# Optimization experiments

Measured on AMD Instinct MI355X. Metric: run time of the kernel, lower is better.

Reference implementation:

```python
import jax
import jax.numpy as jnp
from jax import lax
import numpy as np

# ---- static RPN config (mirrors init_kwargs) ----
STRIDES = (8, 16)
SIZES = ((32, 32), (16, 16))
SCALES = ((64.0 ** 2,), (128.0 ** 2,))
RATIOS = ((0.5, 1.0, 2.0), (0.5, 1.0, 2.0))
IMAGE_SIZE = (256, 256)
NMS_THRESH = 0.7
POST_NMS_TOP_N = 2000
NUM_LEVELS = 2
TOP_K_PER_LEVEL = POST_NMS_TOP_N // NUM_LEVELS  # padded NMS output slots per level


def _generate_anchors(stride, scales, ratios, size, image_size):
    """Anchors of shape (H*W*A, 4) in (x1,y1,x2,y2), clamped to image."""
    H, W = size
    cy = (np.arange(H, dtype=np.float32) + 0.5) * stride
    cx = (np.arange(W, dtype=np.float32) + 0.5) * stride
    ws, hs = [], []
    for s in scales:
        for r in ratios:
            ws.append(np.sqrt(s / r))
            hs.append(np.sqrt(s * r))
    ws = np.asarray(ws, np.float32)  # [A]
    hs = np.asarray(hs, np.float32)
    cxg, cyg = np.meshgrid(cx, cy)  # [H, W]
    x1 = cxg[..., None] - 0.5 * ws
    y1 = cyg[..., None] - 0.5 * hs
    x2 = cxg[..., None] + 0.5 * ws
    y2 = cyg[..., None] + 0.5 * hs
    a = np.stack([x1, y1, x2, y2], axis=-1)  # [H, W, A, 4]
    a[..., 0] = np.clip(a[..., 0], 0, image_size[0])
    a[..., 1] = np.clip(a[..., 1], 0, image_size[1])
    a[..., 2] = np.clip(a[..., 2], 0, image_size[0])
    a[..., 3] = np.clip(a[..., 3], 0, image_size[1])
    return a.reshape(-1, 4).astype(np.float32)


ANCHORS = [
    _generate_anchors(STRIDES[i], SCALES[i], RATIOS[i], SIZES[i], IMAGE_SIZE)
    for i in range(NUM_LEVELS)
]


def conv2d(x, w, b, padding):
    y = lax.conv_general_dilated(
        x, w, window_strides=(1, 1), padding=padding,
        dimension_numbers=("NCHW", "OIHW", "NCHW"))
    return y + b[None, :, None, None]


def decode_boxes(anchors, deltas):
    """Standard R-CNN box decode. anchors [N,4], deltas [..., N, 4]."""
    wa = anchors[:, 2] - anchors[:, 0]
    ha = anchors[:, 3] - anchors[:, 1]
    cxa = anchors[:, 0] + 0.5 * wa
    cya = anchors[:, 1] + 0.5 * ha
    dx, dy, dw, dh = deltas[..., 0], deltas[..., 1], deltas[..., 2], deltas[..., 3]
    cx = dx * wa + cxa
    cy = dy * ha + cya
    w = jnp.exp(dw) * wa
    h = jnp.exp(dh) * ha
    return jnp.stack([cx - 0.5 * w, cy - 0.5 * h, cx + 0.5 * w, cy + 0.5 * h], axis=-1)


def clamp_boxes(b):
    return jnp.stack([
        jnp.clip(b[..., 0], 0.0, IMAGE_SIZE[0]),
        jnp.clip(b[..., 1], 0.0, IMAGE_SIZE[1]),
        jnp.clip(b[..., 2], 0.0, IMAGE_SIZE[0]),
        jnp.clip(b[..., 3], 0.0, IMAGE_SIZE[1]),
    ], axis=-1)


def _pairwise_iou(b):
    # b: [N, 4] -> [N, N] IoU (torchvision convention, no +1)
    area = (b[:, 2] - b[:, 0]) * (b[:, 3] - b[:, 1])
    lt = jnp.maximum(b[:, None, :2], b[None, :, :2])
    rb = jnp.minimum(b[:, None, 2:], b[None, :, 2:])
    wh = jnp.clip(rb - lt, 0.0)
    inter = wh[..., 0] * wh[..., 1]
    return inter / (area[:, None] + area[None, :] - inter)


def nms_padded(boxes, scores, thresh, top_k):
    """Exact greedy NMS; returns (top_k,4) boxes and (top_k,) scores padded with -1."""
    N = boxes.shape[0]
    order = jnp.argsort(-scores)
    b = boxes[order]
    s = scores[order]
    iou = _pairwise_iou(b)  # [N, N]

    def body(supp, xs):
        row, i = xs
        keep_i = jnp.logical_not(supp[i])
        supp = supp | (keep_i & (row > thresh) & (jnp.arange(N) > i))
        return supp, keep_i

    _, keep = lax.scan(body, jnp.zeros((N,), bool), (iou, jnp.arange(N)))
    rank = jnp.cumsum(keep) - 1  # position among kept, in score order
    slot = jnp.where(keep & (rank < top_k), rank, top_k)  # overflow -> dump row
    out_b = jnp.full((top_k + 1, 4), -1.0, boxes.dtype).at[slot].set(b)
    out_s = jnp.full((top_k + 1,), -1.0, scores.dtype).at[slot].set(s)
    return out_b[:top_k], out_s[:top_k]


def _rpn_level(feat, anchors, conv_w, conv_b, cls_w, cls_b, reg_w, reg_b):
    x = jax.nn.relu(conv2d(feat, conv_w, conv_b, "SAME"))
    cls = conv2d(x, cls_w, cls_b, "VALID")              # [BS, A, H, W]
    reg = conv2d(x, reg_w, reg_b, "VALID")              # [BS, 4A, H, W]
    BS, A, H, W = cls.shape
    cls = cls.transpose(0, 2, 3, 1).reshape(BS, -1)                      # [BS, HWA]
    reg = reg.transpose(0, 2, 3, 1).reshape(BS, H, W, A, 4).reshape(BS, -1, 4)
    boxes = clamp_boxes(decode_boxes(anchors, lax.stop_gradient(reg)))   # [BS, HWA, 4]
    scores = jax.nn.sigmoid(lax.stop_gradient(cls))                      # [BS, HWA]
    kb, ks = jax.vmap(lambda bb, ss: nms_padded(bb, ss, NMS_THRESH, TOP_K_PER_LEVEL))(boxes, scores)
    return kb, ks


def setup_inputs() -> dict:
    key = jax.random.key(0)
    ks = jax.random.split(key, 5)
    C = 256
    A = 3
    return {
        "feat0": jax.random.normal(ks[0], (4, C, 32, 32), jnp.float32),
        "feat1": jax.random.normal(ks[1], (4, C, 16, 16), jnp.float32),
        "conv_w": 0.01 * jax.random.normal(ks[2], (C, C, 3, 3), jnp.float32),
        "conv_b": jnp.zeros((C,), jnp.float32),
        "cls_w": 0.01 * jax.random.normal(ks[3], (A, C, 1, 1), jnp.float32),
        "cls_b": jnp.zeros((A,), jnp.float32),
        "reg_w": 0.01 * jax.random.normal(ks[4], (4 * A, C, 1, 1), jnp.float32),
        "reg_b": jnp.zeros((4 * A,), jnp.float32),
    }


def reference(feat0, feat1, conv_w, conv_b, cls_w, cls_b, reg_w, reg_b):
    feats = [feat0, feat1]
    kb_all, ks_all = [], []
    for i in range(NUM_LEVELS):
        kb, ks = _rpn_level(feats[i], jnp.asarray(ANCHORS[i]),
                            conv_w, conv_b, cls_w, cls_b, reg_w, reg_b)
        kb_all.append(kb)
        ks_all.append(ks)
    bboxes = jnp.concatenate(kb_all, axis=1)   # [BS, POST_NMS_TOP_N, 4]
    scores = jnp.concatenate(ks_all, axis=1)   # [BS, POST_NMS_TOP_N]
    idx = jnp.argsort(-scores, axis=1)         # descending; -1 pads go last
    bboxes = jnp.take_along_axis(bboxes, idx[..., None], axis=1)
    return bboxes
```

## Files before the change

kernel.cpp:

```cpp
#include <hip/hip_runtime.h>
#include <math.h>


__global__ __launch_bounds__(256, 4) void conv3_sk_u(
    const float* __restrict__ feat0, const float* __restrict__ feat1,
    const float* __restrict__ conv_w,
    double* __restrict__ part0, double* __restrict__ part1)
{
  __shared__ float Ald[2][16][64];
  __shared__ float Bld[2][16][64];
  const int t = threadIdx.x;
  const int bid = blockIdx.x;
  const float* feat;
  double* part;
  int oc_t, p_t, k_base, hw_sh, w_sh, H;
  if (bid < 1024) {
    int kc = bid >> 8;
    feat = feat0; part = part0 + (size_t)kc * 4096 * 256;
    oc_t = bid & 3; p_t = (bid >> 2) & 63;
    k_base = kc * 576; hw_sh = 10; w_sh = 5; H = 32;
  } else {
    int b2 = bid - 1024;
    int kc = b2 >> 6;
    feat = feat1; part = part1 + (size_t)kc * 1024 * 256;
    oc_t = b2 & 3; p_t = (b2 >> 2) & 15;
    k_base = kc * 576; hw_sh = 8; w_sh = 4; H = 16;
  }
  const int oc_base = oc_t * 64;
  const int p_base  = p_t * 64;
  const int wmask = H - 1, hwmask = (1 << hw_sh) - 1;
  const int skk = t >> 4;
  const int q4  = (t & 15) * 4;

  float a_r[4], b_r[4];
  auto load_tile = [&](int kt) {
    const int k0 = k_base + kt * 16;
    const float* wrow = conv_w + (size_t)(oc_base + q4) * 2304 + (k0 + skk);
#pragma unroll
    for (int u = 0; u < 4; ++u) a_r[u] = wrow[(size_t)u * 2304];
    int p = p_base + q4;
    int b = p >> hw_sh, pin = p & hwmask;
    int y = pin >> w_sh, x0 = pin & wmask;
    int k = k0 + skk;
    int ic = k / 9, rr = k - ic * 9;
    int ky = rr / 3, kx = rr - ky * 3;
    int iy = y + ky - 1;
    const float* frow = feat + (((b << 8) + ic) << hw_sh) + (iy << w_sh);
    bool yok = (unsigned)iy < (unsigned)H;
#pragma unroll
    for (int u = 0; u < 4; ++u) {
      int ix = x0 + u + kx - 1;
      b_r[u] = (yok && (unsigned)ix < (unsigned)H) ? frow[ix] : 0.f;
    }
  };

  const int ty4 = (t >> 4) * 4;
  const int tx4 = (t & 15) * 4;
  double acc[4][4] = {};

  load_tile(0);
  for (int kt = 0; kt < 36; ++kt) {
    const int buf = kt & 1;
    *(float4*)&Ald[buf][skk][q4] = make_float4(a_r[0], a_r[1], a_r[2], a_r[3]);
    *(float4*)&Bld[buf][skk][q4] = make_float4(b_r[0], b_r[1], b_r[2], b_r[3]);
    __syncthreads();
    if (kt + 1 < 36) load_tile(kt + 1);
#pragma unroll
    for (int kk = 0; kk < 16; ++kk) {
      float4 av = *(const float4*)&Ald[buf][kk][ty4];
      float4 bv = *(const float4*)&Bld[buf][kk][tx4];
      double ad[4] = {(double)av.x, (double)av.y, (double)av.z, (double)av.w};
      double bd[4] = {(double)bv.x, (double)bv.y, (double)bv.z, (double)bv.w};
#pragma unroll
      for (int i = 0; i < 4; ++i)
#pragma unroll
        for (int j = 0; j < 4; ++j) acc[i][j] += ad[i] * bd[j];
    }
  }
#pragma unroll
  for (int j = 0; j < 4; ++j) {
    int p = p_base + tx4 + j;
    double* row = part + (size_t)p * 256 + oc_base + ty4;
    *(double2*)&row[0] = make_double2(acc[0][j], acc[1][j]);
    *(double2*)&row[2] = make_double2(acc[2][j], acc[3][j]);
  }
}

__global__ __launch_bounds__(256) void rhd_k(
    const double* __restrict__ part0, const double* __restrict__ part1,
    const float* __restrict__ conv_b,
    const float* __restrict__ cls_w, const float* __restrict__ cls_b,
    const float* __restrict__ reg_w, const float* __restrict__ reg_b,
    float* __restrict__ box0, float* __restrict__ sc0,
    float* __restrict__ box1, float* __restrict__ sc1)
{
  int wid = (blockIdx.x * 256 + threadIdx.x) >> 6;
  int lane = threadIdx.x & 63;
  int lvl = wid >= 4096;
  const double* part = lvl ? part1 : part0;
  int p = lvl ? wid - 4096 : wid;
  int M = lvl ? 1024 : 4096;
  double s4[4];
  {
    float4 bv = ((const float4*)conv_b)[lane];
    s4[0] = (double)bv.x; s4[1] = (double)bv.y;
    s4[2] = (double)bv.z; s4[3] = (double)bv.w;
  }
#pragma unroll
  for (int ks = 0; ks < 4; ++ks) {
    const double2* pr = (const double2*)(part + (size_t)ks * M * 256 + (size_t)p * 256);
    double2 a = pr[2 * lane], b = pr[2 * lane + 1];
    s4[0] += a.x; s4[1] += a.y; s4[2] += b.x; s4[3] += b.y;
  }
  float xv[4];
#pragma unroll
  for (int q = 0; q < 4; ++q) {
    float f = (float)s4[q];
    xv[q] = f > 0.f ? f : 0.f;
  }
  double acc[15];
#pragma unroll
  for (int o = 0; o < 15; ++o) {
    const float* wr = (o < 3) ? (cls_w + o * 256) : (reg_w + (o - 3) * 256);
    float4 wv = ((const float4*)wr)[lane];
    acc[o] = (double)wv.x * (double)xv[0] + (double)wv.y * (double)xv[1] +
             (double)wv.z * (double)xv[2] + (double)wv.w * (double)xv[3];
  }
#pragma unroll
  for (int d = 1; d < 64; d <<= 1)
#pragma unroll
    for (int o = 0; o < 15; ++o)
      acc[o] += __shfl_xor(acc[o], d, 64);
  if (lane < 3) {
    int a = lane;
    float cls = (float)(acc[a] + (double)cls_b[a]);
    float score = 1.f / (1.f + expf(-cls));
    float dx = (float)(acc[3 + a * 4 + 0] + (double)reg_b[a * 4 + 0]);
    float dy = (float)(acc[3 + a * 4 + 1] + (double)reg_b[a * 4 + 1]);
    float dw = (float)(acc[3 + a * 4 + 2] + (double)reg_b[a * 4 + 2]);
    float dh = (float)(acc[3 + a * 4 + 3] + (double)reg_b[a * 4 + 3]);
    int hw_sh = lvl ? 8 : 10, w_sh = lvl ? 4 : 5, Wd = lvl ? 16 : 32;
    float S = lvl ? 16.f : 8.f;
    double scale = lvl ? 16384.0 : 4096.0;
    int b = p >> hw_sh, pin = p & ((1 << hw_sh) - 1);
    int y = pin >> w_sh, x = pin & (Wd - 1);
    double ratio = (a == 0) ? 0.5 : (a == 1 ? 1.0 : 2.0);
    float w_a = (float)sqrt(scale / ratio);
    float h_a = (float)sqrt(scale * ratio);
    float cx = ((float)x + 0.5f) * S;
    float cy = ((float)y + 0.5f) * S;
    float x1 = cx - 0.5f * w_a, y1 = cy - 0.5f * h_a;
    float x2 = cx + 0.5f * w_a, y2 = cy + 0.5f * h_a;
    x1 = fminf(fmaxf(x1, 0.f), 256.f); y1 = fminf(fmaxf(y1, 0.f), 256.f);
    x2 = fminf(fmaxf(x2, 0.f), 256.f); y2 = fminf(fmaxf(y2, 0.f), 256.f);
    float wa = x2 - x1, ha = y2 - y1;
    float cxa = x1 + 0.5f * wa, cya = y1 + 0.5f * ha;
    float ncx = dx * wa + cxa;
    float ncy = dy * ha + cya;
    float nw = expf(dw) * wa;
    float nh = expf(dh) * ha;
    float bx1 = ncx - 0.5f * nw, by1 = ncy - 0.5f * nh;
    float bx2 = ncx + 0.5f * nw, by2 = ncy + 0.5f * nh;
    bx1 = fminf(fmaxf(bx1, 0.f), 256.f); by1 = fminf(fmaxf(by1, 0.f), 256.f);
    bx2 = fminf(fmaxf(bx2, 0.f), 256.f); by2 = fminf(fmaxf(by2, 0.f), 256.f);
    int n = pin * 3 + a;
    if (lvl) {
      ((float4*)box1)[(size_t)b * 768 + n] = make_float4(bx1, by1, bx2, by2);
      sc1[b * 768 + n] = score;
    } else {
      ((float4*)box0)[(size_t)b * 3072 + n] = make_float4(bx1, by1, bx2, by2);
      sc0[b * 3072 + n] = score;
    }
  }
}

__global__ __launch_bounds__(256) void sort_level_k(
    const float* __restrict__ sc0, const float* __restrict__ box0,
    float* __restrict__ ssc0, float* __restrict__ sbox0,
    const float* __restrict__ sc1, const float* __restrict__ box1,
    float* __restrict__ ssc1, float* __restrict__ sbox1)
{
  __shared__ __align__(16) float s[3072];
  int z = blockIdx.x;
  const float *sc, *box; float *ssc, *sbox; int N, b, c;
  if (z < 48) { sc = sc0; box = box0; ssc = ssc0; sbox = sbox0; N = 3072; b = z / 12; c = z % 12; }
  else { int z2 = z - 48; sc = sc1; box = box1; ssc = ssc1; sbox = sbox1; N = 768; b = z2 / 3; c = z2 % 3; }
  const float* scb = sc + (size_t)b * N;
  for (int j = threadIdx.x; j < N; j += 256) s[j] = scb[j];
  __syncthreads();
  int i = c * 256 + threadIdx.x;
  float si = s[i];
  int rank = 0;
  const float4* sv = (const float4*)s;
  for (int j4 = 0; j4 < (N >> 2); ++j4) {
    float4 v = sv[j4];
    int j = j4 * 4;
    rank += (v.x > si) || (v.x == si && (j + 0) < i);
    rank += (v.y > si) || (v.y == si && (j + 1) < i);
    rank += (v.z > si) || (v.z == si && (j + 2) < i);
    rank += (v.w > si) || (v.w == si && (j + 3) < i);
  }
  ssc[(size_t)b * N + rank] = si;
  float4 bi = ((const float4*)box)[(size_t)b * N + i];
  ((float4*)sbox)[(size_t)b * N + rank] = bi;
}

__global__ __launch_bounds__(256) void mask_col_k(
    const float* __restrict__ sbox0, const float* __restrict__ sbox1,
    unsigned long long* __restrict__ mask0, unsigned long long* __restrict__ mask1,
    unsigned long long* __restrict__ colD0, unsigned long long* __restrict__ colD1)
{
  int bid = blockIdx.x;
  if (bid < 2448) {
    __shared__ float4 bj[64];
    const float* sbox; unsigned long long* mask; int N, words, w, i_ch, b;
    if (bid < 2304) {
      sbox = sbox0; mask = mask0; N = 3072; words = 48;
      w = bid % 48; int r = bid / 48; i_ch = r % 12; b = r / 12;
    } else {
      int z = bid - 2304;
      sbox = sbox1; mask = mask1; N = 768; words = 12;
      w = z % 12; int r = z / 12; i_ch = r % 3; b = r / 3;
    }
    int i = i_ch * 256 + threadIdx.x;
    if (threadIdx.x < 64)
      bj[threadIdx.x] = ((const float4*)sbox)[(size_t)b * N + w * 64 + threadIdx.x];
    __syncthreads();
    float4 bi = ((const float4*)sbox)[(size_t)b * N + i];
    float ai = (bi.z - bi.x) * (bi.w - bi.y);
    unsigned long long m = 0ull;
#pragma unroll 16
    for (int jj = 0; jj < 64; ++jj) {
      int j = w * 64 + jj;
      float4 bv = bj[jj];
      float lx = fmaxf(bi.x, bv.x), ly = fmaxf(bi.y, bv.y);
      float rx = fminf(bi.z, bv.z), ry = fminf(bi.w, bv.w);
      float iw = fmaxf(rx - lx, 0.f), ih = fmaxf(ry - ly, 0.f);
      float inter = iw * ih;
      float aj = (bv.z - bv.x) * (bv.w - bv.y);
      float iou = inter / (ai + aj - inter);
      if ((iou > 0.7f) & (j > i)) m |= (1ull << jj);
    }
    mask[((size_t)b * N + i) * words + w] = m;
  } else {
    __shared__ float4 tb[4][64];
    int sub = threadIdx.x >> 6, lane = threadIdx.x & 63;
    const float* sbox; unsigned long long* colD; int N, tile, b;
    if (bid < 2496) {
      int unit = (bid - 2448) * 4 + sub;
      sbox = sbox0; colD = colD0; N = 3072;
      tile = unit % 48; b = unit / 48;
    } else {
      int unit = (bid - 2496) * 4 + sub;
      sbox = sbox1; colD = colD1; N = 768;
      tile = unit % 12; b = unit / 12;
    }
    tb[sub][lane] = ((const float4*)sbox)[(size_t)b * N + tile * 64 + lane];
    __syncthreads();
    float4 bq = tb[sub][lane];
    float aq = (bq.z - bq.x) * (bq.w - bq.y);
    unsigned long long col = 0ull;
#pragma unroll 16
    for (int ii = 0; ii < 64; ++ii) {
      float4 bi = tb[sub][ii];
      float lx = fmaxf(bq.x, bi.x), ly = fmaxf(bq.y, bi.y);
      float rx = fminf(bq.z, bi.z), ry = fminf(bq.w, bi.w);
      float iw = fmaxf(rx - lx, 0.f), ih = fmaxf(ry - ly, 0.f);
      float inter = iw * ih;
      float ai = (bi.z - bi.x) * (bi.w - bi.y);
      float iou = inter / (aq + ai - inter);
      if ((iou > 0.7f) & (lane > ii)) col |= (1ull << ii);
    }
    colD[(size_t)b * N + tile * 64 + lane] = col;
  }
}

__global__ __launch_bounds__(64) void nms_scan_k(
    const float* __restrict__ ssc0, const float* __restrict__ sbox0,
    const unsigned long long* __restrict__ mask0,
    const unsigned long long* __restrict__ colD0,
    const float* __restrict__ ssc1, const float* __restrict__ sbox1,
    const unsigned long long* __restrict__ mask1,
    const unsigned long long* __restrict__ colD1,
    float* __restrict__ cb, float* __restrict__ cs)
{
  int z = blockIdx.x;
  int lvl = z >> 2, b = z & 3;
  int N = lvl ? 768 : 3072;
  int words = lvl ? 12 : 48;
  const float* ssc = (lvl ? ssc1 : ssc0) + (size_t)b * N;
  const float4* sbox = ((const float4*)(lvl ? sbox1 : sbox0)) + (size_t)b * N;
  const unsigned long long* mask = (lvl ? mask1 : mask0) + (size_t)b * N * words;
  const unsigned long long* colD = (lvl ? colD1 : colD0) + (size_t)b * N;
  const int lane = threadIdx.x;
  float* csb = cs + (size_t)b * 2000 + lvl * 1000;
  float4* cbb = (float4*)(cb + ((size_t)b * 2000 + lvl * 1000) * 4);
  for (int q = lane; q < 1000; q += 64) {
    csb[q] = -1.f;
    cbb[q] = make_float4(-1.f, -1.f, -1.f, -1.f);
  }
  unsigned long long removed = 0ull;
  int kept_base = 0;
  unsigned long long colv = colD[lane];
  float sc_i = ssc[lane];
  float4 bx_i = sbox[lane];
  for (int t = 0; t < words; ++t) {
    unsigned long long wr = __shfl(removed, t);
    bool doprop = (lane > t) && (lane < words);
    const unsigned long long* row = mask + (size_t)t * 64 * words + lane;
    unsigned long long v1[32], v2[32];
    if (doprop) {
#pragma unroll
      for (int s = 0; s < 32; ++s) v1[s] = row[(size_t)s * words];
#pragma unroll
      for (int s = 0; s < 32; ++s) v2[s] = row[(size_t)(32 + s) * words];
    }
    bool rm = (wr >> lane) & 1ull;
    bool kp = false;
    unsigned long long Rv = wr;
    unsigned long long Kv = 0ull;
    while (true) {
      bool F = (!rm) && (!kp) && ((colv & ~Rv) == 0ull);
      unsigned long long Fv = __ballot(F);
      if (Fv == 0ull) break;
      kp = kp || F;
      Kv |= Fv;
      bool newr = (!rm) && (!kp) && ((colv & Fv) != 0ull);
      rm = rm || newr;
      Rv = __ballot(rm);
    }
    unsigned long long keep64 = Kv;
    if (kp) {
      int rank = kept_base + __popcll(keep64 & ((1ull << lane) - 1ull));
      if (rank < 1000) { csb[rank] = sc_i; cbb[rank] = bx_i; }
    }
    kept_base += __popcll(keep64);
    if (kept_base >= 1000) break;
    if (t + 1 >= words) break;
    {
      int i2 = (t + 1) * 64 + lane;
      colv = colD[i2]; sc_i = ssc[i2]; bx_i = sbox[i2];
    }
    if (doprop) {
      unsigned long long acc = removed;
#pragma unroll
      for (int s = 0; s < 32; ++s)
        acc |= (((keep64 >> s) & 1ull) ? v1[s] : 0ull);
#pragma unroll
      for (int s = 0; s < 32; ++s)
        acc |= (((keep64 >> (32 + s)) & 1ull) ? v2[s] : 0ull);
      removed = acc;
    }
  }
}

__global__ __launch_bounds__(256) void final_sort_k(
    const float* __restrict__ cs, const float* __restrict__ cb,
    float* __restrict__ out)
{
  __shared__ __align__(16) float s[2000];
  int b = blockIdx.x >> 3, c = blockIdx.x & 7;
  const float* csb = cs + (size_t)b * 2000;
  for (int j = threadIdx.x; j < 2000; j += 256) s[j] = csb[j];
  __syncthreads();
  if (threadIdx.x >= 250) return;
  int li = c * 250 + threadIdx.x;
  float si = s[li];
  int rank = 0;
  const float4* sv = (const float4*)s;
  for (int j4 = 0; j4 < 500; ++j4) {
    float4 v = sv[j4];
    int j = j4 * 4;
    rank += (v.x > si) || (v.x == si && (j + 0) < li);
    rank += (v.y > si) || (v.y == si && (j + 1) < li);
    rank += (v.z > si) || (v.z == si && (j + 2) < li);
    rank += (v.w > si) || (v.w == si && (j + 3) < li);
  }
  float4 bi = ((const float4*)cb)[(size_t)b * 2000 + li];
  ((float4*)out)[(size_t)b * 2000 + rank] = bi;
}

extern "C" void kernel_launch(void* const* d_in, const int* in_sizes, int n_in,
                              void* d_out, int out_size, void* d_ws, size_t ws_size,
                              hipStream_t stream) {
  const float* feat0  = (const float*)d_in[0];
  const float* feat1  = (const float*)d_in[1];
  const float* conv_w = (const float*)d_in[2];
  const float* conv_b = (const float*)d_in[3];
  const float* cls_w  = (const float*)d_in[4];
  const float* cls_b  = (const float*)d_in[5];
  const float* reg_w  = (const float*)d_in[6];
  const float* reg_b  = (const float*)d_in[7];

  char* p = (char*)d_ws;
  auto alloc = [&](size_t bytes) {
    char* r = p;
    p += (bytes + 255) & ~(size_t)255;
    return r;
  };
  double* part0 = (double*)alloc((size_t)4 * 4096 * 256 * 8);
  double* part1 = (double*)alloc((size_t)4 * 1024 * 256 * 8);
  float* box0 = (float*)alloc((size_t)4 * 3072 * 16);
  float* sc0  = (float*)alloc((size_t)4 * 3072 * 4);
  float* box1 = (float*)alloc((size_t)4 * 768 * 16);
  float* sc1  = (float*)alloc((size_t)4 * 768 * 4);
  float* sbox0 = (float*)alloc((size_t)4 * 3072 * 16);
  float* ssc0  = (float*)alloc((size_t)4 * 3072 * 4);
  float* sbox1 = (float*)alloc((size_t)4 * 768 * 16);
  float* ssc1  = (float*)alloc((size_t)4 * 768 * 4);
  unsigned long long* mask0 = (unsigned long long*)alloc((size_t)4 * 3072 * 48 * 8);
  unsigned long long* mask1 = (unsigned long long*)alloc((size_t)4 * 768 * 12 * 8);
  unsigned long long* colD0 = (unsigned long long*)alloc((size_t)4 * 3072 * 8);
  unsigned long long* colD1 = (unsigned long long*)alloc((size_t)4 * 768 * 8);
  float* cb = (float*)alloc((size_t)4 * 2000 * 16);
  float* cs = (float*)alloc((size_t)4 * 2000 * 4);

  conv3_sk_u<<<1280, 256, 0, stream>>>(feat0, feat1, conv_w, part0, part1);
  rhd_k<<<1280, 256, 0, stream>>>(part0, part1, conv_b, cls_w, cls_b,
                                  reg_w, reg_b, box0, sc0, box1, sc1);
  sort_level_k<<<60, 256, 0, stream>>>(sc0, box0, ssc0, sbox0,
                                       sc1, box1, ssc1, sbox1);
  mask_col_k<<<2508, 256, 0, stream>>>(sbox0, sbox1, mask0, mask1, colD0, colD1);
  nms_scan_k<<<8, 64, 0, stream>>>(ssc0, sbox0, mask0, colD0,
                                   ssc1, sbox1, mask1, colD1, cb, cs);
  final_sort_k<<<32, 256, 0, stream>>>(cs, cb, (float*)d_out);
}
```

Baseline: 533.2 us.

## Fuse post-conv stages into one persistent kernel with grid barriers

Merges the head, per-level sort, IoU mask, NMS scan and final sort kernels into a single persistent kernel of 512 blocks, separated by software grid barriers built on atomics. The aim is to remove per-kernel launch overhead and the gaps between the five small dependent launches. In exchange it adds a memset and barrier spin costs. It also relies on all 512 blocks being resident at once (launch bounds 256,2), since otherwise the barrier deadlocks. The NMS scan now loads its mask rows in two halves to reduce register use.

```diff
diff --git a/kernel.cpp b/kernel.cpp
--- a/kernel.cpp
+++ b/kernel.cpp
@@ -86,298 +86,305 @@
   }
 }
 
-__global__ __launch_bounds__(256) void rhd_k(
+#define POST_NBLK 512
+__device__ __forceinline__ void grid_barrier(int* cnt, int* gen) {
+  __syncthreads();
+  if (threadIdx.x == 0) {
+    __threadfence();
+    int g = atomicAdd(gen, 0);
+    if (atomicAdd(cnt, 1) == POST_NBLK - 1) {
+      atomicExch(cnt, 0);
+      __threadfence();
+      atomicAdd(gen, 1);
+    } else {
+      while (atomicAdd(gen, 0) == g) { __builtin_amdgcn_s_sleep(8); }
+    }
+    __threadfence();
+  }
+  __syncthreads();
+}
+
+__global__ __launch_bounds__(256, 2) void post_k(
     const double* __restrict__ part0, const double* __restrict__ part1,
     const float* __restrict__ conv_b,
     const float* __restrict__ cls_w, const float* __restrict__ cls_b,
     const float* __restrict__ reg_w, const float* __restrict__ reg_b,
-    float* __restrict__ box0, float* __restrict__ sc0,
-    float* __restrict__ box1, float* __restrict__ sc1)
+    float* box0, float* sc0, float* box1, float* sc1,
+    float* ssc0, float* sbox0, float* ssc1, float* sbox1,
+    unsigned long long* mask0, unsigned long long* mask1,
+    unsigned long long* colD0, unsigned long long* colD1,
+    float* cb, float* cs, float* out, int* bar)
 {
-  int wid = (blockIdx.x * 256 + threadIdx.x) >> 6;
-  int lane = threadIdx.x & 63;
-  int lvl = wid >= 4096;
-  const double* part = lvl ? part1 : part0;
-  int p = lvl ? wid - 4096 : wid;
-  int M = lvl ? 1024 : 4096;
-  double s4[4];
-  {
-    float4 bv = ((const float4*)conv_b)[lane];
-    s4[0] = (double)bv.x; s4[1] = (double)bv.y;
-    s4[2] = (double)bv.z; s4[3] = (double)bv.w;
-  }
-#pragma unroll
-  for (int ks = 0; ks < 4; ++ks) {
-    const double2* pr = (const double2*)(part + (size_t)ks * M * 256 + (size_t)p * 256);
-    double2 a = pr[2 * lane], b = pr[2 * lane + 1];
-    s4[0] += a.x; s4[1] += a.y; s4[2] += b.x; s4[3] += b.y;
-  }
-  float xv[4];
-#pragma unroll
-  for (int q = 0; q < 4; ++q) {
-    float f = (float)s4[q];
-    xv[q] = f > 0.f ? f : 0.f;
-  }
-  double acc[15];
-#pragma unroll
-  for (int o = 0; o < 15; ++o) {
-    const float* wr = (o < 3) ? (cls_w + o * 256) : (reg_w + (o - 3) * 256);
-    float4 wv = ((const float4*)wr)[lane];
-    acc[o] = (double)wv.x * (double)xv[0] + (double)wv.y * (double)xv[1] +
-             (double)wv.z * (double)xv[2] + (double)wv.w * (double)xv[3];
-  }
-#pragma unroll
-  for (int d = 1; d < 64; d <<= 1)
-#pragma unroll
-    for (int o = 0; o < 15; ++o)
-      acc[o] += __shfl_xor(acc[o], d, 64);
-  if (lane < 3) {
-    int a = lane;
-    float cls = (float)(acc[a] + (double)cls_b[a]);
-    float score = 1.f / (1.f + expf(-cls));
-    float dx = (float)(acc[3 + a * 4 + 0] + (double)reg_b[a * 4 + 0]);
-    float dy = (float)(acc[3 + a * 4 + 1] + (double)reg_b[a * 4 + 1]);
-    float dw = (float)(acc[3 + a * 4 + 2] + (double)reg_b[a * 4 + 2]);
-    float dh = (float)(acc[3 + a * 4 + 3] + (double)reg_b[a * 4 + 3]);
-    int hw_sh = lvl ? 8 : 10, w_sh = lvl ? 4 : 5, Wd = lvl ? 16 : 32;
-    float S = lvl ? 16.f : 8.f;
-    double scale = lvl ? 16384.0 : 4096.0;
-    int b = p >> hw_sh, pin = p & ((1 << hw_sh) - 1);
-    int y = pin >> w_sh, x = pin & (Wd - 1);
-    double ratio = (a == 0) ? 0.5 : (a == 1 ? 1.0 : 2.0);
-    float w_a = (float)sqrt(scale / ratio);
-    float h_a = (float)sqrt(scale * ratio);
-    float cx = ((float)x + 0.5f) * S;
-    float cy = ((float)y + 0.5f) * S;
-    float x1 = cx - 0.5f * w_a, y1 = cy - 0.5f * h_a;
-    float x2 = cx + 0.5f * w_a, y2 = cy + 0.5f * h_a;
-    x1 = fminf(fmaxf(x1, 0.f), 256.f); y1 = fminf(fmaxf(y1, 0.f), 256.f);
-    x2 = fminf(fmaxf(x2, 0.f), 256.f); y2 = fminf(fmaxf(y2, 0.f), 256.f);
-    float wa = x2 - x1, ha = y2 - y1;
-    float cxa = x1 + 0.5f * wa, cya = y1 + 0.5f * ha;
-    float ncx = dx * wa + cxa;
-    float ncy = dy * ha + cya;
-    float nw = expf(dw) * wa;
-    float nh = expf(dh) * ha;
-    float bx1 = ncx - 0.5f * nw, by1 = ncy - 0.5f * nh;
-    float bx2 = ncx + 0.5f * nw, by2 = ncy + 0.5f * nh;
-    bx1 = fminf(fmaxf(bx1, 0.f), 256.f); by1 = fminf(fmaxf(by1, 0.f), 256.f);
-    bx2 = fminf(fmaxf(bx2, 0.f), 256.f); by2 = fminf(fmaxf(by2, 0.f), 256.f);
-    int n = pin * 3 + a;
-    if (lvl) {
-      ((float4*)box1)[(size_t)b * 768 + n] = make_float4(bx1, by1, bx2, by2);
-      sc1[b * 768 + n] = score;
+  int* bcnt = bar;
+  int* bgen = bar + 1;
+  __shared__ __align__(16) float smem[3072];
+  const int bid = blockIdx.x;
+  const int tid = threadIdx.x;
+  const int lane = tid & 63;
+
+  for (int u = bid * 4 + (tid >> 6); u < 5120; u += 2048) {
+    int lvl = u >= 4096;
+    const double* part = lvl ? part1 : part0;
+    int p = lvl ? u - 4096 : u;
+    int M = lvl ? 1024 : 4096;
+    double s4[4];
+    {
+      float4 bv = ((const float4*)conv_b)[lane];
+      s4[0] = (double)bv.x; s4[1] = (double)bv.y;
+      s4[2] = (double)bv.z; s4[3] = (double)bv.w;
+    }
+#pragma unroll
+    for (int ks = 0; ks < 4; ++ks) {
+      const double2* pr = (const double2*)(part + (size_t)ks * M * 256 + (size_t)p * 256);
+      double2 a = pr[2 * lane], b = pr[2 * lane + 1];
+      s4[0] += a.x; s4[1] += a.y; s4[2] += b.x; s4[3] += b.y;
+    }
+    float xv[4];
+#pragma unroll
+    for (int q = 0; q < 4; ++q) {
+      float f = (float)s4[q];
+      xv[q] = f > 0.f ? f : 0.f;
+    }
+    double acc[15];
+#pragma unroll
+    for (int o = 0; o < 15; ++o) {
+      const float* wr = (o < 3) ? (cls_w + o * 256) : (reg_w + (o - 3) * 256);
+      float4 wv = ((const float4*)wr)[lane];
+      acc[o] = (double)wv.x * (double)xv[0] + (double)wv.y * (double)xv[1] +
+               (double)wv.z * (double)xv[2] + (double)wv.w * (double)xv[3];
+    }
+#pragma unroll
+    for (int d = 1; d < 64; d <<= 1)
+#pragma unroll
+      for (int o = 0; o < 15; ++o)
+        acc[o] += __shfl_xor(acc[o], d, 64);
+    if (lane < 3) {
+      int a = lane;
+      float cls = (float)(acc[a] + (double)cls_b[a]);
+      float score = 1.f / (1.f + expf(-cls));
+      float dx = (float)(acc[3 + a * 4 + 0] + (double)reg_b[a * 4 + 0]);
+      float dy = (float)(acc[3 + a * 4 + 1] + (double)reg_b[a * 4 + 1]);
+      float dw = (float)(acc[3 + a * 4 + 2] + (double)reg_b[a * 4 + 2]);
+      float dh = (float)(acc[3 + a * 4 + 3] + (double)reg_b[a * 4 + 3]);
+      int hw_sh = lvl ? 8 : 10, w_sh = lvl ? 4 : 5, Wd = lvl ? 16 : 32;
+      float S = lvl ? 16.f : 8.f;
+      double scale = lvl ? 16384.0 : 4096.0;
+      int b = p >> hw_sh, pin = p & ((1 << hw_sh) - 1);
+      int y = pin >> w_sh, x = pin & (Wd - 1);
+      double ratio = (a == 0) ? 0.5 : (a == 1 ? 1.0 : 2.0);
+      float w_a = (float)sqrt(scale / ratio);
+      float h_a = (float)sqrt(scale * ratio);
+      float cx = ((float)x + 0.5f) * S;
+      float cy = ((float)y + 0.5f) * S;
+      float x1 = cx - 0.5f * w_a, y1 = cy - 0.5f * h_a;
+      float x2 = cx + 0.5f * w_a, y2 = cy + 0.5f * h_a;
+      x1 = fminf(fmaxf(x1, 0.f), 256.f); y1 = fminf(fmaxf(y1, 0.f), 256.f);
+      x2 = fminf(fmaxf(x2, 0.f), 256.f); y2 = fminf(fmaxf(y2, 0.f), 256.f);
+      float wa = x2 - x1, ha = y2 - y1;
+      float cxa = x1 + 0.5f * wa, cya = y1 + 0.5f * ha;
+      float ncx = dx * wa + cxa;
+      float ncy = dy * ha + cya;
+      float nw = expf(dw) * wa;
+      float nh = expf(dh) * ha;
+      float bx1 = ncx - 0.5f * nw, by1 = ncy - 0.5f * nh;
+      float bx2 = ncx + 0.5f * nw, by2 = ncy + 0.5f * nh;
+      bx1 = fminf(fmaxf(bx1, 0.f), 256.f); by1 = fminf(fmaxf(by1, 0.f), 256.f);
+      bx2 = fminf(fmaxf(bx2, 0.f), 256.f); by2 = fminf(fmaxf(by2, 0.f), 256.f);
+      int n = pin * 3 + a;
+      if (lvl) {
+        ((float4*)box1)[(size_t)b * 768 + n] = make_float4(bx1, by1, bx2, by2);
+        sc1[b * 768 + n] = score;
+      } else {
+        ((float4*)box0)[(size_t)b * 3072 + n] = make_float4(bx1, by1, bx2, by2);
+        sc0[b * 3072 + n] = score;
+      }
+    }
+  }
+  grid_barrier(bcnt, bgen);
+
+  if (bid < 60) {
+    const float *sc, *box; float *ssc, *sbox; int N, b, c;
+    if (bid < 48) { sc = sc0; box = box0; ssc = ssc0; sbox = sbox0; N = 3072; b = bid / 12; c = bid % 12; }
+    else { int z2 = bid - 48; sc = sc1; box = box1; ssc = ssc1; sbox = sbox1; N = 768; b = z2 / 3; c = z2 % 3; }
+    const float* scb = sc + (size_t)b * N;
+    for (int j = tid; j < N; j += 256) smem[j] = scb[j];
+    __syncthreads();
+    int i = c * 256 + tid;
+    float si = smem[i];
+    int rank = 0;
+    const float4* sv = (const float4*)smem;
+    for (int j4 = 0; j4 < (N >> 2); ++j4) {
+      float4 v = sv[j4];
+      int j = j4 * 4;
+      rank += (v.x > si) || (v.x == si && (j + 0) < i);
+      rank += (v.y > si) || (v.y == si && (j + 1) < i);
+      rank += (v.z > si) || (v.z == si && (j + 2) < i);
+      rank += (v.w > si) || (v.w == si && (j + 3) < i);
+    }
+    ssc[(size_t)b * N + rank] = si;
+    float4 bi = ((const float4*)box)[(size_t)b * N + i];
+    ((float4*)sbox)[(size_t)b * N + rank] = bi;
+  }
+  grid_barrier(bcnt, bgen);
+
+  for (int u = bid; u < 2508; u += 512) {
+    __syncthreads();
+    float4* f4 = (float4*)smem;
+    if (u < 2448) {
+      const float* sbox; unsigned long long* mask; int N, words, w, i_ch, b;
+      if (u < 2304) {
+        sbox = sbox0; mask = mask0; N = 3072; words = 48;
+        w = u % 48; int r = u / 48; i_ch = r % 12; b = r / 12;
+      } else {
+        int z = u - 2304;
+        sbox = sbox1; mask = mask1; N = 768; words = 12;
+        w = z % 12; int r = z / 12; i_ch = r % 3; b = r / 3;
+      }
+      int i = i_ch * 256 + tid;
+      if (tid < 64)
+        f4[tid] = ((const float4*)sbox)[(size_t)b * N + w * 64 + tid];
+      __syncthreads();
+      float4 bi = ((const float4*)sbox)[(size_t)b * N + i];
+      float ai = (bi.z - bi.x) * (bi.w - bi.y);
+      unsigned long long m = 0ull;
+#pragma unroll 16
+      for (int jj = 0; jj < 64; ++jj) {
+        int j = w * 64 + jj;
+        float4 bv = f4[jj];
+        float lx = fmaxf(bi.x, bv.x), ly = fmaxf(bi.y, bv.y);
+        float rx = fminf(bi.z, bv.z), ry = fminf(bi.w, bv.w);
+        float iw = fmaxf(rx - lx, 0.f), ih = fmaxf(ry - ly, 0.f);
+        float inter = iw * ih;
+        float aj = (bv.z - bv.x) * (bv.w - bv.y);
+        float iou = inter / (ai + aj - inter);
+        if ((iou > 0.7f) & (j > i)) m |= (1ull << jj);
+      }
+      mask[((size_t)b * N + i) * words + w] = m;
     } else {
-      ((float4*)box0)[(size_t)b * 3072 + n] = make_float4(bx1, by1, bx2, by2);
-      sc0[b * 3072 + n] = score;
-    }
-  }
-}
-
-__global__ __launch_bounds__(256) void sort_level_k(
-    const float* __restrict__ sc0, const float* __restrict__ box0,
-    float* __restrict__ ssc0, float* __restrict__ sbox0,
-    const float* __restrict__ sc1, const float* __restrict__ box1,
-    float* __restrict__ ssc1, float* __restrict__ sbox1)
-{
-  __shared__ __align__(16) float s[3072];
-  int z = blockIdx.x;
-  const float *sc, *box; float *ssc, *sbox; int N, b, c;
-  if (z < 48) { sc = sc0; box = box0; ssc = ssc0; sbox = sbox0; N = 3072; b = z / 12; c = z % 12; }
-  else { int z2 = z - 48; sc = sc1; box = box1; ssc = ssc1; sbox = sbox1; N = 768; b = z2 / 3; c = z2 % 3; }
-  const float* scb = sc + (size_t)b * N;
-  for (int j = threadIdx.x; j < N; j += 256) s[j] = scb[j];
-  __syncthreads();
-  int i = c * 256 + threadIdx.x;
-  float si = s[i];
-  int rank = 0;
-  const float4* sv = (const float4*)s;
-  for (int j4 = 0; j4 < (N >> 2); ++j4) {
-    float4 v = sv[j4];
-    int j = j4 * 4;
-    rank += (v.x > si) || (v.x == si && (j + 0) < i);
-    rank += (v.y > si) || (v.y == si && (j + 1) < i);
-    rank += (v.z > si) || (v.z == si && (j + 2) < i);
-    rank += (v.w > si) || (v.w == si && (j + 3) < i);
-  }
-  ssc[(size_t)b * N + rank] = si;
-  float4 bi = ((const float4*)box)[(size_t)b * N + i];
-  ((float4*)sbox)[(size_t)b * N + rank] = bi;
-}
-
-__global__ __launch_bounds__(256) void mask_col_k(
-    const float* __restrict__ sbox0, const float* __restrict__ sbox1,
-    unsigned long long* __restrict__ mask0, unsigned long long* __restrict__ mask1,
-    unsigned long long* __restrict__ colD0, unsigned long long* __restrict__ colD1)
-{
-  int bid = blockIdx.x;
-  if (bid < 2448) {
-    __shared__ float4 bj[64];
-    const float* sbox; unsigned long long* mask; int N, words, w, i_ch, b;
-    if (bid < 2304) {
-      sbox = sbox0; mask = mask0; N = 3072; words = 48;
-      w = bid % 48; int r = bid / 48; i_ch = r % 12; b = r / 12;
-    } else {
-      int z = bid - 2304;
-      sbox = sbox1; mask = mask1; N = 768; words = 12;
-      w = z % 12; int r = z / 12; i_ch = r % 3; b = r / 3;
-    }
-    int i = i_ch * 256 + threadIdx.x;
-    if (threadIdx.x < 64)
-      bj[threadIdx.x] = ((const float4*)sbox)[(size_t)b * N + w * 64 + threadIdx.x];
+      int sub = tid >> 6;
+      const float* sbox; unsigned long long* colD; int N, tile, b;
+      if (u < 2496) {
+        int unit = (u - 2448) * 4 + sub;
+        sbox = sbox0; colD = colD0; N = 3072;
+        tile = unit % 48; b = unit / 48;
+      } else {
+        int unit = (u - 2496) * 4 + sub;
+        sbox = sbox1; colD = colD1; N = 768;
+        tile = unit % 12; b = unit / 12;
+      }
+      f4[sub * 64 + lane] = ((const float4*)sbox)[(size_t)b * N + tile * 64 + lane];
+      __syncthreads();
+      float4 bq = f4[sub * 64 + lane];
+      float aq = (bq.z - bq.x) * (bq.w - bq.y);
+      unsigned long long col = 0ull;
+#pragma unroll 16
+      for (int ii = 0; ii < 64; ++ii) {
+        float4 bi = f4[sub * 64 + ii];
+        float lx = fmaxf(bq.x, bi.x), ly = fmaxf(bq.y, bi.y);
+        float rx = fminf(bq.z, bi.z), ry = fminf(bq.w, bi.w);
+        float iw = fmaxf(rx - lx, 0.f), ih = fmaxf(ry - ly, 0.f);
+        float inter = iw * ih;
+        float ai = (bi.z - bi.x) * (bi.w - bi.y);
+        float iou = inter / (aq + ai - inter);
+        if ((iou > 0.7f) & (lane > ii)) col |= (1ull << ii);
+      }
+      colD[(size_t)b * N + tile * 64 + lane] = col;
+    }
+  }
+  grid_barrier(bcnt, bgen);
+
+  if (bid < 8 && tid < 64) {
+    int lvl = bid >> 2, b = bid & 3;
+    int N = lvl ? 768 : 3072;
+    int words = lvl ? 12 : 48;
+    const float* ssc = (lvl ? ssc1 : ssc0) + (size_t)b * N;
+    const float4* sbox = ((const float4*)(lvl ? sbox1 : sbox0)) + (size_t)b * N;
+    const unsigned long long* mask = (lvl ? mask1 : mask0) + (size_t)b * N * words;
+    const unsigned long long* colD = (lvl ? colD1 : colD0) + (size_t)b * N;
+    float* csb = cs + (size_t)b * 2000 + lvl * 1000;
+    float4* cbb = (float4*)(cb + ((size_t)b * 2000 + lvl * 1000) * 4);
+    for (int q = lane; q < 1000; q += 64) {
+      csb[q] = -1.f;
+      cbb[q] = make_float4(-1.f, -1.f, -1.f, -1.f);
+    }
+    unsigned long long removed = 0ull;
+    int kept_base = 0;
+    unsigned long long colv = colD[lane];
+    float sc_i = ssc[lane];
+    float4 bx_i = sbox[lane];
+    for (int t = 0; t < words; ++t) {
+      unsigned long long wr = __shfl(removed, t);
+      bool doprop = (lane > t) && (lane < words);
+      const unsigned long long* row = mask + (size_t)t * 64 * words + lane;
+      unsigned long long v[32];
+      if (doprop) {
+#pragma unroll
+        for (int s = 0; s < 32; ++s) v[s] = row[(size_t)s * words];
+      }
+      bool rm = (wr >> lane) & 1ull;
+      bool kp = false;
+      unsigned long long Rv = wr;
+      unsigned long long Kv = 0ull;
+      while (true) {
+        bool F = (!rm) && (!kp) && ((colv & ~Rv) == 0ull);
+        unsigned long long Fv = __ballot(F);
+        if (Fv == 0ull) break;
+        kp = kp || F;
+        Kv |= Fv;
+        bool newr = (!rm) && (!kp) && ((colv & Fv) != 0ull);
+        rm = rm || newr;
+        Rv = __ballot(rm);
+      }
+      unsigned long long keep64 = Kv;
+      if (kp) {
+        int rank = kept_base + __popcll(keep64 & ((1ull << lane) - 1ull));
+        if (rank < 1000) { csb[rank] = sc_i; cbb[rank] = bx_i; }
+      }
+      kept_base += __popcll(keep64);
+      if (kept_base >= 1000) break;
+      if (t + 1 >= words) break;
+      {
+        int i2 = (t + 1) * 64 + lane;
+        colv = colD[i2]; sc_i = ssc[i2]; bx_i = sbox[i2];
+      }
+      if (doprop) {
+        unsigned long long acc = removed;
+#pragma unroll
+        for (int s = 0; s < 32; ++s)
+          acc |= (((keep64 >> s) & 1ull) ? v[s] : 0ull);
+#pragma unroll
+        for (int s = 0; s < 32; ++s) v[s] = row[(size_t)(32 + s) * words];
+#pragma unroll
+        for (int s = 0; s < 32; ++s)
+          acc |= (((keep64 >> (32 + s)) & 1ull) ? v[s] : 0ull);
+        removed = acc;
+      }
+    }
+  }
+  grid_barrier(bcnt, bgen);
+
+  if (bid < 32) {
+    int b = bid >> 3, c = bid & 7;
+    const float* csb = cs + (size_t)b * 2000;
+    for (int j = tid; j < 2000; j += 256) smem[j] = csb[j];
     __syncthreads();
-    float4 bi = ((const float4*)sbox)[(size_t)b * N + i];
-    float ai = (bi.z - bi.x) * (bi.w - bi.y);
-    unsigned long long m = 0ull;
-#pragma unroll 16
-    for (int jj = 0; jj < 64; ++jj) {
-      int j = w * 64 + jj;
-      float4 bv = bj[jj];
-      float lx = fmaxf(bi.x, bv.x), ly = fmaxf(bi.y, bv.y);
-      float rx = fminf(bi.z, bv.z), ry = fminf(bi.w, bv.w);
-      float iw = fmaxf(rx - lx, 0.f), ih = fmaxf(ry - ly, 0.f);
-      float inter = iw * ih;
-      float aj = (bv.z - bv.x) * (bv.w - bv.y);
-      float iou = inter / (ai + aj - inter);
-      if ((iou > 0.7f) & (j > i)) m |= (1ull << jj);
-    }
-    mask[((size_t)b * N + i) * words + w] = m;
-  } else {
-    __shared__ float4 tb[4][64];
-    int sub = threadIdx.x >> 6, lane = threadIdx.x & 63;
-    const float* sbox; unsigned long long* colD; int N, tile, b;
-    if (bid < 2496) {
-      int unit = (bid - 2448) * 4 + sub;
-      sbox = sbox0; colD = colD0; N = 3072;
-      tile = unit % 48; b = unit / 48;
-    } else {
-      int unit = (bid - 2496) * 4 + sub;
-      sbox = sbox1; colD = colD1; N = 768;
-      tile = unit % 12; b = unit / 12;
-    }
-    tb[sub][lane] = ((const float4*)sbox)[(size_t)b * N + tile * 64 + lane];
-    __syncthreads();
-    float4 bq = tb[sub][lane];
-    float aq = (bq.z - bq.x) * (bq.w - bq.y);
-    unsigned long long col = 0ull;
-#pragma unroll 16
-    for (int ii = 0; ii < 64; ++ii) {
-      float4 bi = tb[sub][ii];
-      float lx = fmaxf(bq.x, bi.x), ly = fmaxf(bq.y, bi.y);
-      float rx = fminf(bq.z, bi.z), ry = fminf(bq.w, bi.w);
-      float iw = fmaxf(rx - lx, 0.f), ih = fmaxf(ry - ly, 0.f);
-      float inter = iw * ih;
-      float ai = (bi.z - bi.x) * (bi.w - bi.y);
-      float iou = inter / (aq + ai - inter);
-      if ((iou > 0.7f) & (lane > ii)) col |= (1ull << ii);
-    }
-    colD[(size_t)b * N + tile * 64 + lane] = col;
-  }
-}
-
-__global__ __launch_bounds__(64) void nms_scan_k(
-    const float* __restrict__ ssc0, const float* __restrict__ sbox0,
-    const unsigned long long* __restrict__ mask0,
-    const unsigned long long* __restrict__ colD0,
-    const float* __restrict__ ssc1, const float* __restrict__ sbox1,
-    const unsigned long long* __restrict__ mask1,
-    const unsigned long long* __restrict__ colD1,
-    float* __restrict__ cb, float* __restrict__ cs)
-{
-  int z = blockIdx.x;
-  int lvl = z >> 2, b = z & 3;
-  int N = lvl ? 768 : 3072;
-  int words = lvl ? 12 : 48;
-  const float* ssc = (lvl ? ssc1 : ssc0) + (size_t)b * N;
-  const float4* sbox = ((const float4*)(lvl ? sbox1 : sbox0)) + (size_t)b * N;
-  const unsigned long long* mask = (lvl ? mask1 : mask0) + (size_t)b * N * words;
-  const unsigned long long* colD = (lvl ? colD1 : colD0) + (size_t)b * N;
-  const int lane = threadIdx.x;
-  float* csb = cs + (size_t)b * 2000 + lvl * 1000;
-  float4* cbb = (float4*)(cb + ((size_t)b * 2000 + lvl * 1000) * 4);
-  for (int q = lane; q < 1000; q += 64) {
-    csb[q] = -1.f;
-    cbb[q] = make_float4(-1.f, -1.f, -1.f, -1.f);
-  }
-  unsigned long long removed = 0ull;
-  int kept_base = 0;
-  unsigned long long colv = colD[lane];
-  float sc_i = ssc[lane];
-  float4 bx_i = sbox[lane];
-  for (int t = 0; t < words; ++t) {
-    unsigned long long wr = __shfl(removed, t);
-    bool doprop = (lane > t) && (lane < words);
-    const unsigned long long* row = mask + (size_t)t * 64 * words + lane;
-    unsigned long long v1[32], v2[32];
-    if (doprop) {
-#pragma unroll
-      for (int s = 0; s < 32; ++s) v1[s] = row[(size_t)s * words];
-#pragma unroll
-      for (int s = 0; s < 32; ++s) v2[s] = row[(size_t)(32 + s) * words];
-    }
-    bool rm = (wr >> lane) & 1ull;
-    bool kp = false;
-    unsigned long long Rv = wr;
-    unsigned long long Kv = 0ull;
-    while (true) {
-      bool F = (!rm) && (!kp) && ((colv & ~Rv) == 0ull);
-      unsigned long long Fv = __ballot(F);
-      if (Fv == 0ull) break;
-      kp = kp || F;
-      Kv |= Fv;
-      bool newr = (!rm) && (!kp) && ((colv & Fv) != 0ull);
-      rm = rm || newr;
-      Rv = __ballot(rm);
-    }
-    unsigned long long keep64 = Kv;
-    if (kp) {
-      int rank = kept_base + __popcll(keep64 & ((1ull << lane) - 1ull));
-      if (rank < 1000) { csb[rank] = sc_i; cbb[rank] = bx_i; }
-    }
-    kept_base += __popcll(keep64);
-    if (kept_base >= 1000) break;
-    if (t + 1 >= words) break;
-    {
-      int i2 = (t + 1) * 64 + lane;
-      colv = colD[i2]; sc_i = ssc[i2]; bx_i = sbox[i2];
-    }
-    if (doprop) {
-      unsigned long long acc = removed;
-#pragma unroll
-      for (int s = 0; s < 32; ++s)
-        acc |= (((keep64 >> s) & 1ull) ? v1[s] : 0ull);
-#pragma unroll
-      for (int s = 0; s < 32; ++s)
-        acc |= (((keep64 >> (32 + s)) & 1ull) ? v2[s] : 0ull);
-      removed = acc;
-    }
-  }
-}
-
-__global__ __launch_bounds__(256) void final_sort_k(
-    const float* __restrict__ cs, const float* __restrict__ cb,
-    float* __restrict__ out)
-{
-  __shared__ __align__(16) float s[2000];
-  int b = blockIdx.x >> 3, c = blockIdx.x & 7;
-  const float* csb = cs + (size_t)b * 2000;
-  for (int j = threadIdx.x; j < 2000; j += 256) s[j] = csb[j];
-  __syncthreads();
-  if (threadIdx.x >= 250) return;
-  int li = c * 250 + threadIdx.x;
-  float si = s[li];
-  int rank = 0;
-  const float4* sv = (const float4*)s;
-  for (int j4 = 0; j4 < 500; ++j4) {
-    float4 v = sv[j4];
-    int j = j4 * 4;
-    rank += (v.x > si) || (v.x == si && (j + 0) < li);
-    rank += (v.y > si) || (v.y == si && (j + 1) < li);
-    rank += (v.z > si) || (v.z == si && (j + 2) < li);
-    rank += (v.w > si) || (v.w == si && (j + 3) < li);
-  }
-  float4 bi = ((const float4*)cb)[(size_t)b * 2000 + li];
-  ((float4*)out)[(size_t)b * 2000 + rank] = bi;
+    if (tid < 250) {
+      int li = c * 250 + tid;
+      float si = smem[li];
+      int rank = 0;
+      const float4* sv = (const float4*)smem;
+      for (int j4 = 0; j4 < 500; ++j4) {
+        float4 v = sv[j4];
+        int j = j4 * 4;
+        rank += (v.x > si) || (v.x == si && (j + 0) < li);
+        rank += (v.y > si) || (v.y == si && (j + 1) < li);
+        rank += (v.z > si) || (v.z == si && (j + 2) < li);
+        rank += (v.w > si) || (v.w == si && (j + 3) < li);
+      }
+      float4 bi = ((const float4*)cb)[(size_t)b * 2000 + li];
+      ((float4*)out)[(size_t)b * 2000 + rank] = bi;
+    }
+  }
 }
 
 extern "C" void kernel_launch(void* const* d_in, const int* in_sizes, int n_in,
@@ -414,14 +421,13 @@
   unsigned long long* colD1 = (unsigned long long*)alloc((size_t)4 * 768 * 8);
   float* cb = (float*)alloc((size_t)4 * 2000 * 16);
   float* cs = (float*)alloc((size_t)4 * 2000 * 4);
+  int* bar = (int*)alloc(256);
+  float* outp = (float*)d_out;
 
   conv3_sk_u<<<1280, 256, 0, stream>>>(feat0, feat1, conv_w, part0, part1);
-  rhd_k<<<1280, 256, 0, stream>>>(part0, part1, conv_b, cls_w, cls_b,
-                                  reg_w, reg_b, box0, sc0, box1, sc1);
-  sort_level_k<<<60, 256, 0, stream>>>(sc0, box0, ssc0, sbox0,
-                                       sc1, box1, ssc1, sbox1);
-  mask_col_k<<<2508, 256, 0, stream>>>(sbox0, sbox1, mask0, mask1, colD0, colD1);
-  nms_scan_k<<<8, 64, 0, stream>>>(ssc0, sbox0, mask0, colD0,
-                                   ssc1, sbox1, mask1, colD1, cb, cs);
-  final_sort_k<<<32, 256, 0, stream>>>(cs, cb, (float*)d_out);
+  hipMemsetAsync(bar, 0, 8, stream);
+  post_k<<<POST_NBLK, 256, 0, stream>>>(
+      part0, part1, conv_b, cls_w, cls_b, reg_w, reg_b,
+      box0, sc0, box1, sc1, ssc0, sbox0, ssc1, sbox1,
+      mask0, mask1, colD0, colD1, cb, cs, outp, bar);
 }
```

Result: slower. 697.6 us (+30.8%).

## Split NMS mask propagation across four waves with shared-memory reduction

Applied to the files above, without the earlier changes.

The serial NMS scan kernel now runs 256 threads per block instead of one 64-lane wave. Each wave loads 16 of the 64 mask rows per tile, so per-thread register pressure and load latency drop. Wave 0 alone runs the greedy keep/remove ballot loop. All waves then OR their partial suppression masks into shared memory, which adds three block barriers per tile in exchange for spreading the mask loads.

```diff
diff --git a/kernel.cpp b/kernel.cpp
--- a/kernel.cpp
+++ b/kernel.cpp
@@ -275,7 +275,7 @@
   }
 }
 
-__global__ __launch_bounds__(64) void nms_scan_k(
+__global__ __launch_bounds__(256) void nms_scan_k(
     const float* __restrict__ ssc0, const float* __restrict__ sbox0,
     const unsigned long long* __restrict__ mask0,
     const unsigned long long* __restrict__ colD0,
@@ -292,65 +292,81 @@
   const float4* sbox = ((const float4*)(lvl ? sbox1 : sbox0)) + (size_t)b * N;
   const unsigned long long* mask = (lvl ? mask1 : mask0) + (size_t)b * N * words;
   const unsigned long long* colD = (lvl ? colD1 : colD0) + (size_t)b * N;
-  const int lane = threadIdx.x;
+  const int tid = threadIdx.x;
+  const int lane = tid & 63;
+  const int wv = tid >> 6;
   float* csb = cs + (size_t)b * 2000 + lvl * 1000;
   float4* cbb = (float4*)(cb + ((size_t)b * 2000 + lvl * 1000) * 4);
-  for (int q = lane; q < 1000; q += 64) {
+
+  __shared__ unsigned long long rem[48];
+  __shared__ unsigned long long part[4][64];
+  __shared__ unsigned long long keepSh;
+  __shared__ int doneSh;
+
+  if (tid < 48) rem[tid] = 0ull;
+  if (tid == 0) doneSh = 0;
+  for (int q = tid; q < 1000; q += 256) {
     csb[q] = -1.f;
     cbb[q] = make_float4(-1.f, -1.f, -1.f, -1.f);
   }
-  unsigned long long removed = 0ull;
+  unsigned long long colv = 0ull; float sc_i = 0.f; float4 bx_i;
+  if (wv == 0) { colv = colD[lane]; sc_i = ssc[lane]; bx_i = sbox[lane]; }
   int kept_base = 0;
-  unsigned long long colv = colD[lane];
-  float sc_i = ssc[lane];
-  float4 bx_i = sbox[lane];
+  __syncthreads();
+
   for (int t = 0; t < words; ++t) {
-    unsigned long long wr = __shfl(removed, t);
-    bool doprop = (lane > t) && (lane < words);
-    const unsigned long long* row = mask + (size_t)t * 64 * words + lane;
-    unsigned long long v1[32], v2[32];
-    if (doprop) {
-#pragma unroll
-      for (int s = 0; s < 32; ++s) v1[s] = row[(size_t)s * words];
-#pragma unroll
-      for (int s = 0; s < 32; ++s) v2[s] = row[(size_t)(32 + s) * words];
-    }
-    bool rm = (wr >> lane) & 1ull;
-    bool kp = false;
-    unsigned long long Rv = wr;
-    unsigned long long Kv = 0ull;
-    while (true) {
-      bool F = (!rm) && (!kp) && ((colv & ~Rv) == 0ull);
-      unsigned long long Fv = __ballot(F);
-      if (Fv == 0ull) break;
-      kp = kp || F;
-      Kv |= Fv;
-      bool newr = (!rm) && (!kp) && ((colv & Fv) != 0ull);
-      rm = rm || newr;
-      Rv = __ballot(rm);
-    }
-    unsigned long long keep64 = Kv;
-    if (kp) {
-      int rank = kept_base + __popcll(keep64 & ((1ull << lane) - 1ull));
-      if (rank < 1000) { csb[rank] = sc_i; cbb[rank] = bx_i; }
-    }
-    kept_base += __popcll(keep64);
-    if (kept_base >= 1000) break;
-    if (t + 1 >= words) break;
-    {
-      int i2 = (t + 1) * 64 + lane;
-      colv = colD[i2]; sc_i = ssc[i2]; bx_i = sbox[i2];
-    }
-    if (doprop) {
-      unsigned long long acc = removed;
-#pragma unroll
-      for (int s = 0; s < 32; ++s)
-        acc |= (((keep64 >> s) & 1ull) ? v1[s] : 0ull);
-#pragma unroll
-      for (int s = 0; s < 32; ++s)
-        acc |= (((keep64 >> (32 + s)) & 1ull) ? v2[s] : 0ull);
-      removed = acc;
-    }
+    unsigned long long v[16];
+    if (lane < words) {
+      const unsigned long long* rowb =
+          mask + ((size_t)t * 64 + wv * 16) * words + lane;
+#pragma unroll
+      for (int s = 0; s < 16; ++s) v[s] = rowb[(size_t)s * words];
+    }
+    if (wv == 0) {
+      unsigned long long wr = rem[t];
+      bool rm = (wr >> lane) & 1ull;
+      bool kp = false;
+      unsigned long long Rv = wr;
+      unsigned long long Kv = 0ull;
+      while (true) {
+        bool F = (!rm) && (!kp) && ((colv & ~Rv) == 0ull);
+        unsigned long long Fv = __ballot(F);
+        if (Fv == 0ull) break;
+        kp = kp || F;
+        Kv |= Fv;
+        bool newr = (!rm) && (!kp) && ((colv & Fv) != 0ull);
+        rm = rm || newr;
+        Rv = __ballot(rm);
+      }
+      if (kp) {
+        int rank = kept_base + __popcll(Kv & ((1ull << lane) - 1ull));
+        if (rank < 1000) { csb[rank] = sc_i; cbb[rank] = bx_i; }
+      }
+      kept_base += __popcll(Kv);
+      if (lane == 0) {
+        keepSh = Kv;
+        doneSh = (kept_base >= 1000 || t + 1 >= words) ? 1 : 0;
+      }
+      if (t + 1 < words) {
+        int i2 = (t + 1) * 64 + lane;
+        colv = colD[i2]; sc_i = ssc[i2]; bx_i = sbox[i2];
+      }
+    }
+    __syncthreads();
+    unsigned long long k64 = keepSh;
+    int done = doneSh;
+    if (lane < words) {
+      unsigned long long acc = 0ull;
+#pragma unroll
+      for (int s = 0; s < 16; ++s)
+        acc |= (((k64 >> (wv * 16 + s)) & 1ull) ? v[s] : 0ull);
+      part[wv][lane] = acc;
+    }
+    __syncthreads();
+    if (done) break;
+    if (tid > t && tid < words)
+      rem[tid] |= part[0][tid] | part[1][tid] | part[2][tid] | part[3][tid];
+    __syncthreads();
   }
 }
 
@@ -421,7 +437,7 @@
   sort_level_k<<<60, 256, 0, stream>>>(sc0, box0, ssc0, sbox0,
                                        sc1, box1, ssc1, sbox1);
   mask_col_k<<<2508, 256, 0, stream>>>(sbox0, sbox1, mask0, mask1, colD0, colD1);
-  nms_scan_k<<<8, 64, 0, stream>>>(ssc0, sbox0, mask0, colD0,
-                                   ssc1, sbox1, mask1, colD1, cb, cs);
+  nms_scan_k<<<8, 256, 0, stream>>>(ssc0, sbox0, mask0, colD0,
+                                    ssc1, sbox1, mask1, colD1, cb, cs);
   final_sort_k<<<32, 256, 0, stream>>>(cs, cb, (float*)d_out);
 }
```

Result: faster. 492.5 us (median of 2 runs) (-7.6%).
